# Performance work log

Measured on AMD Instinct MI355X. Metric: run time of the kernel, lower is better.

The kernel has to match this reference:

```python
import jax, jax.numpy as jnp
import numpy as np

B, T, IN, H, L, OUT = 2048, 512, 4, 64, 4, 5


def setup_inputs() -> dict:
    key = jax.random.key(0)
    ks = jax.random.split(key, 9)
    s = 0.1  # keep gates out of saturation
    return {
        "x": jax.random.normal(ks[0], (B, T, IN), jnp.float32),
        "W_ih0": jax.random.normal(ks[1], (4 * H, IN), jnp.float32) * s,
        "W_ih_r": jax.random.normal(ks[2], (L - 1, 4 * H, H), jnp.float32) * s,
        "W_hh": jax.random.normal(ks[3], (L, 4 * H, H), jnp.float32) * s,
        "b_ih": jax.random.normal(ks[4], (L, 4 * H), jnp.float32) * s,
        "b_hh": jax.random.normal(ks[5], (L, 4 * H), jnp.float32) * s,
        "W_fc": jax.random.normal(ks[6], (OUT, H), jnp.float32) * s,
        "b_fc": jax.random.normal(ks[7], (OUT,), jnp.float32) * s,
    }


def _lstm_layer(xs, W_ih, W_hh, b_ih, b_hh):
    # xs: [B, T, D_in] -> hs: [B, T, H]. PyTorch gate order: i, f, g, o.
    b, t = xs.shape[0], xs.shape[1]
    h_dim = W_hh.shape[1]
    # Precompute input contribution for all timesteps (one big GEMM).
    xg = jnp.einsum('btd,gd->btg', xs, W_ih) + b_ih  # [B, T, 4H]

    def step(carry, xg_t):
        h, c = carry
        g = xg_t + h @ W_hh.T + b_hh  # [B, 4H]
        i, f, gg, o = jnp.split(g, 4, axis=-1)
        c = jax.nn.sigmoid(f) * c + jax.nn.sigmoid(i) * jnp.tanh(gg)
        h = jax.nn.sigmoid(o) * jnp.tanh(c)
        return (h, c), h

    init = (jnp.zeros((b, h_dim), xs.dtype), jnp.zeros((b, h_dim), xs.dtype))
    (_, _), hs = jax.lax.scan(step, init, jnp.swapaxes(xg, 0, 1))  # hs: [T, B, H]
    return jnp.swapaxes(hs, 0, 1)


def reference(x, W_ih0, W_ih_r, W_hh, b_ih, b_hh, W_fc, b_fc):
    hs = _lstm_layer(x, W_ih0, W_hh[0], b_ih[0], b_hh[0])
    for l in range(1, L):
        hs = _lstm_layer(hs, W_ih_r[l - 1], W_hh[l], b_ih[l], b_hh[l])
    # fc on last timestep of top layer
    return hs[:, -1, :] @ W_fc.T + b_fc  # [B, OUT]
```

## Files before the change

kernel.cpp:

```cpp
#include <hip/hip_runtime.h>


#define B_    2048
#define T_    512
#define H_    64
#define OUT_  5
#define RSTR  136
#define LOG2E 1.44269504088896340736f

typedef _Float16 f16;
typedef __attribute__((ext_vector_type(8))) _Float16 f16x8;
typedef __attribute__((ext_vector_type(4))) float f32x4;

__device__ __forceinline__ float rcpf(float v) { return __builtin_amdgcn_rcpf(v); }
__device__ __forceinline__ float ex2(float v)  { return __builtin_amdgcn_exp2f(v); }

__global__ __launch_bounds__(1024, 4) void lstm_ring_k(
    const float* __restrict__ x,
    const float* __restrict__ W_ih0,
    const float* __restrict__ W_ihr,
    const float* __restrict__ W_hh,
    const float* __restrict__ b_ih,
    const float* __restrict__ b_hh,
    const float* __restrict__ W_fc,
    const float* __restrict__ b_fc,
    float* __restrict__ out)
{
    const int tid  = threadIdx.x;
    const int wave = tid >> 6;
    const int l    = wave >> 2;
    const int jj   = wave & 3;
    const int lane = tid & 63;
    const int q    = lane >> 4;
    const int ln   = lane & 15;
    const int u    = jj * 16 + ln;
    const int b0   = blockIdx.x * 8;

    __shared__ f16 buf[4][4][16][RSTR];
    __shared__ int flg[16];
    __shared__ float hf[8][H_ + 1];

    for (int k = tid; k < (int)(sizeof(buf) / 4); k += 1024) ((unsigned*)buf)[k] = 0u;
    if (tid < 16) flg[tid] = 0;

    const float* Whh = W_hh + (size_t)l * 256 * 64;
    const float* Wih = (l == 0) ? W_ih0 : (W_ihr + (size_t)(l - 1) * 256 * 64);
    const float scg[4] = {-LOG2E, -LOG2E, 2.0f * LOG2E, -LOG2E};

    f16x8 Wf[4][4];
    float biasv[4];
#pragma unroll
    for (int g4 = 0; g4 < 4; ++g4) {
        const int n = g4 * 64 + u;
        biasv[g4] = (b_ih[l * 256 + n] + b_hh[l * 256 + n]) * scg[g4];
#pragma unroll
        for (int kt = 0; kt < 4; ++kt) {
            f16x8 f;
#pragma unroll
            for (int e = 0; e < 8; ++e) {
                const int kap = kt * 32 + q * 8 + e;
                float wv;
                if (kap < 64) {
                    const int k = ((kap & 3) << 4) | (kap >> 2);
                    wv = Whh[n * 64 + k];
                } else {
                    const int kk = kap - 64;
                    if (l == 0) wv = (kk < 4) ? Wih[n * 4 + kk] : 0.0f;
                    else { const int k = ((kk & 3) << 4) | (kk >> 2); wv = Wih[n * 64 + k]; }
                }
                f[e] = (f16)(wv * scg[g4]);
            }
            Wf[g4][kt] = f;
        }
    }

    int fIdx = 0, fOff = 0;
    bool fUse = false;
    if (lane < 3)                             { fIdx = 4 * l + ((jj + 1 + lane) & 3); fOff = 0;  fUse = true; }
    else if (lane >= 3 && lane < 7 && l > 0)  { fIdx = 4 * (l - 1) + (lane - 3);      fOff = 1;  fUse = true; }
    else if (lane >= 7 && lane < 11 && l < 3) { fIdx = 4 * (l + 1) + (lane - 7);      fOff = -3; fUse = true; }

    const int l1 = (l < 3) ? l + 1 : 3;
    const int rdOff = ln * RSTR;
    const int owOff = 4 * q * RSTR + 4 * ln + jj;
    const int inOff = 4 * q * RSTR + 64 + 4 * ln + jj;

    const int xm = lane >> 2, xe = lane & 3;
    const int xrow = 4 * (xm >> 1) + (xm & 1);
    const bool xldr = (wave == 0 && lane < 32);
    float xA = 0.0f;

    __syncthreads();
    if (xldr) {
        const float x0 = x[(size_t)(b0 + xm) * (T_ * 4) + xe];
        buf[0][0][xrow][64 + xe] = (f16)x0;
        xA = x[(size_t)(b0 + xm) * (T_ * 4) + 4 + xe];
    }
    __syncthreads();

    const f32x4 Z0 = {0.f, 0.f, 0.f, 0.f};
    float cst[2] = {0.f, 0.f};

    auto body = [&](int t, int sl) {
        const int sn = (sl + 1) & 3;
        unsigned guard = 0;
        for (;;) {
            int v = 0x7fffffff;
            if (fUse) v = __hip_atomic_load(&flg[fIdx], __ATOMIC_ACQUIRE,
                                            __HIP_MEMORY_SCOPE_WORKGROUP);
            if (__all(v >= t + fOff)) break;
            if (++guard > 2) __builtin_amdgcn_s_sleep(1);
            if (guard > (1u << 16)) break;
        }

        const f16* rb = &buf[l][sl][0][0] + rdOff;
        f16x8 A[4];
#pragma unroll
        for (int kt = 0; kt < 4; ++kt)
            A[kt] = *(const f16x8*)(rb + kt * 32 + q * 8);

        f32x4 acc[4];
#pragma unroll
        for (int g4 = 0; g4 < 4; ++g4)
            acc[g4] = __builtin_amdgcn_mfma_f32_16x16x32_f16(A[0], Wf[g4][0], Z0, 0, 0, 0);
#pragma unroll
        for (int kt = 1; kt < 4; ++kt)
#pragma unroll
            for (int g4 = 0; g4 < 4; ++g4)
                acc[g4] = __builtin_amdgcn_mfma_f32_16x16x32_f16(A[kt], Wf[g4][kt], acc[g4], 0, 0, 0);

        if (xldr) {
            if (t + 1 < T_) buf[0][sn][xrow][64 + xe] = (f16)xA;
            if (t + 2 < T_) xA = x[(size_t)(b0 + xm) * (T_ * 4) + (t + 2) * 4 + xe];
        }

        f16* wO = &buf[l][sn][0][0] + owOff;
        f16* wI = &buf[l1][sl][0][0] + inOff;
#pragma unroll
        for (int rr = 0; rr < 2; ++rr) {
            const float si = rcpf(1.0f + ex2(acc[0][rr] + biasv[0]));
            const float sf = rcpf(1.0f + ex2(acc[1][rr] + biasv[1]));
            const float tg = 1.0f - 2.0f * rcpf(1.0f + ex2(acc[2][rr] + biasv[2]));
            const float so = rcpf(1.0f + ex2(acc[3][rr] + biasv[3]));
            const float c  = sf * cst[rr] + si * tg;
            cst[rr] = c;
            const float tc = 1.0f - 2.0f * rcpf(1.0f + ex2(c * (2.0f * LOG2E)));
            const float h  = so * tc;
            wO[rr * RSTR] = (f16)h;
            if (l < 3) wI[rr * RSTR] = (f16)h;
            if (l == 3 && t == T_ - 1) hf[2 * q + rr][u] = h;
        }

        if (lane == 0)
            __hip_atomic_store(&flg[wave], t + 1, __ATOMIC_RELEASE,
                               __HIP_MEMORY_SCOPE_WORKGROUP);
    };

#pragma unroll 1
    for (int t = 0; t < T_; t += 4) {
        body(t, 0);
        body(t + 1, 1);
        body(t + 2, 2);
        body(t + 3, 3);
    }

    __syncthreads();
    if (tid < 8 * OUT_) {
        const int b = tid / OUT_, o = tid % OUT_;
        float a = b_fc[o];
#pragma unroll
        for (int k = 0; k < H_; ++k)
            a = fmaf(hf[b][k], W_fc[o * H_ + k], a);
        out[(b0 + b) * OUT_ + o] = a;
    }
}

extern "C" void kernel_launch(void* const* d_in, const int* in_sizes, int n_in,
                              void* d_out, int out_size, void* d_ws, size_t ws_size,
                              hipStream_t stream) {
    const float* x     = (const float*)d_in[0];
    const float* W_ih0 = (const float*)d_in[1];
    const float* W_ihr = (const float*)d_in[2];
    const float* W_hh  = (const float*)d_in[3];
    const float* b_ih  = (const float*)d_in[4];
    const float* b_hh  = (const float*)d_in[5];
    const float* W_fc  = (const float*)d_in[6];
    const float* b_fc  = (const float*)d_in[7];
    float* out = (float*)d_out;

    lstm_ring_k<<<dim3(B_ / 8), dim3(1024), 0, stream>>>(
        x, W_ih0, W_ihr, W_hh, b_ih, b_hh, W_fc, b_fc, out);
}
```

Before: 602.9 us.

## Replace flag-based layer ring with skewed wavefront using block barriers

Replaces per-wave atomic flag spinning with a diagonal (skewed) schedule where layer l processes timestep i-l and all waves synchronize with __syncthreads each step, double-buffering hidden state per layer. The whole x sequence for the block is preloaded into LDS as fp16 up front, and layer 0 skips the fourth MFMA k-tile since its input has only 4 features. This aims to remove spin-wait and atomic overhead and per-step global x loads, at the cost of a full workgroup barrier every step, 3 extra pipeline fill/drain steps, and larger LDS usage that may reduce occupancy.

```diff
diff --git a/kernel.cpp b/kernel.cpp
--- a/kernel.cpp
+++ b/kernel.cpp
@@ -5,17 +5,18 @@
 #define T_    512
 #define H_    64
 #define OUT_  5
-#define RSTR  136
+#define RSTR  72
 #define LOG2E 1.44269504088896340736f
 
 typedef _Float16 f16;
+typedef __attribute__((ext_vector_type(4))) _Float16 f16x4;
 typedef __attribute__((ext_vector_type(8))) _Float16 f16x8;
 typedef __attribute__((ext_vector_type(4))) float f32x4;
 
 __device__ __forceinline__ float rcpf(float v) { return __builtin_amdgcn_rcpf(v); }
 __device__ __forceinline__ float ex2(float v)  { return __builtin_amdgcn_exp2f(v); }
 
-__global__ __launch_bounds__(1024, 4) void lstm_ring_k(
+__global__ __launch_bounds__(1024, 4) void lstm_skew_k(
     const float* __restrict__ x,
     const float* __restrict__ W_ih0,
     const float* __restrict__ W_ihr,
@@ -36,12 +37,20 @@
     const int u    = jj * 16 + ln;
     const int b0   = blockIdx.x * 8;
 
-    __shared__ f16 buf[4][4][16][RSTR];
-    __shared__ int flg[16];
+    __shared__ f16  buf[4][2][16][RSTR];
+    __shared__ f16  xlds[T_ * 32];
     __shared__ float hf[8][H_ + 1];
 
     for (int k = tid; k < (int)(sizeof(buf) / 4); k += 1024) ((unsigned*)buf)[k] = 0u;
-    if (tid < 16) flg[tid] = 0;
+
+#pragma unroll
+    for (int k = 0; k < 4; ++k) {
+        const int idx = tid + k * 1024;
+        const int bb  = idx >> 9, tt = idx & 511;
+        const float4 v = *(const float4*)(x + (size_t)(b0 + bb) * (T_ * 4) + tt * 4);
+        f16x4 h4; h4[0] = (f16)v.x; h4[1] = (f16)v.y; h4[2] = (f16)v.z; h4[3] = (f16)v.w;
+        *(f16x4*)&xlds[tt * 32 + bb * 4] = h4;
+    }
 
     const float* Whh = W_hh + (size_t)l * 256 * 64;
     const float* Wih = (l == 0) ? W_ih0 : (W_ihr + (size_t)(l - 1) * 256 * 64);
@@ -74,97 +83,82 @@
         }
     }
 
-    int fIdx = 0, fOff = 0;
-    bool fUse = false;
-    if (lane < 3)                             { fIdx = 4 * l + ((jj + 1 + lane) & 3); fOff = 0;  fUse = true; }
-    else if (lane >= 3 && lane < 7 && l > 0)  { fIdx = 4 * (l - 1) + (lane - 3);      fOff = 1;  fUse = true; }
-    else if (lane >= 7 && lane < 11 && l < 3) { fIdx = 4 * (l + 1) + (lane - 7);      fOff = -3; fUse = true; }
+    const int rdOff = ln * RSTR;
+    const f16* hRd0 = &buf[l][0][0][0] + rdOff;
+    const f16* hRd1 = &buf[l][1][0][0] + rdOff;
+    const int  lp   = (l > 0) ? (l - 1) : 0;
+    const f16* iRd0 = &buf[lp][0][0][0] + rdOff;
+    const f16* iRd1 = &buf[lp][1][0][0] + rdOff;
+    const int owOff = 4 * q * RSTR + 4 * ln + jj;
+    f16* hWr0 = &buf[l][0][0][0] + owOff;
+    f16* hWr1 = &buf[l][1][0][0] + owOff;
 
-    const int l1 = (l < 3) ? l + 1 : 3;
-    const int rdOff = ln * RSTR;
-    const int owOff = 4 * q * RSTR + 4 * ln + jj;
-    const int inOff = 4 * q * RSTR + 64 + 4 * ln + jj;
+    const int  xb  = 2 * (ln >> 2) + (ln & 1);
+    const bool xok = (l == 0) && (q == 0) && ((ln & 2) == 0);
+    const f16* xP  = &xlds[xb * 4];
 
-    const int xm = lane >> 2, xe = lane & 3;
-    const int xrow = 4 * (xm >> 1) + (xm & 1);
-    const bool xldr = (wave == 0 && lane < 32);
-    float xA = 0.0f;
-
-    __syncthreads();
-    if (xldr) {
-        const float x0 = x[(size_t)(b0 + xm) * (T_ * 4) + xe];
-        buf[0][0][xrow][64 + xe] = (f16)x0;
-        xA = x[(size_t)(b0 + xm) * (T_ * 4) + 4 + xe];
-    }
     __syncthreads();
 
     const f32x4 Z0 = {0.f, 0.f, 0.f, 0.f};
     float cst[2] = {0.f, 0.f};
 
-    auto body = [&](int t, int sl) {
-        const int sn = (sl + 1) & 3;
-        unsigned guard = 0;
-        for (;;) {
-            int v = 0x7fffffff;
-            if (fUse) v = __hip_atomic_load(&flg[fIdx], __ATOMIC_ACQUIRE,
-                                            __HIP_MEMORY_SCOPE_WORKGROUP);
-            if (__all(v >= t + fOff)) break;
-            if (++guard > 2) __builtin_amdgcn_s_sleep(1);
-            if (guard > (1u << 16)) break;
-        }
+    auto step = [&](const int i, const f16* hb, const f16* ib, f16* wOb) {
+        const int t = i - l;
+        if ((unsigned)t < T_) {
+            f16x8 A0 = *(const f16x8*)(hb + q * 8);
+            f16x8 A1 = *(const f16x8*)(hb + 32 + q * 8);
+            f16x8 A2;
+            if (l == 0) {
+#pragma unroll
+                for (int e = 0; e < 8; ++e) A2[e] = (f16)0;
+                if (xok) {
+                    const f16x4 xv = *(const f16x4*)(xP + t * 32);
+                    A2[0] = xv[0]; A2[1] = xv[1]; A2[2] = xv[2]; A2[3] = xv[3];
+                }
+            } else {
+                A2 = *(const f16x8*)(ib + q * 8);
+            }
 
-        const f16* rb = &buf[l][sl][0][0] + rdOff;
-        f16x8 A[4];
-#pragma unroll
-        for (int kt = 0; kt < 4; ++kt)
-            A[kt] = *(const f16x8*)(rb + kt * 32 + q * 8);
-
-        f32x4 acc[4];
-#pragma unroll
-        for (int g4 = 0; g4 < 4; ++g4)
-            acc[g4] = __builtin_amdgcn_mfma_f32_16x16x32_f16(A[0], Wf[g4][0], Z0, 0, 0, 0);
-#pragma unroll
-        for (int kt = 1; kt < 4; ++kt)
+            f32x4 acc[4];
 #pragma unroll
             for (int g4 = 0; g4 < 4; ++g4)
-                acc[g4] = __builtin_amdgcn_mfma_f32_16x16x32_f16(A[kt], Wf[g4][kt], acc[g4], 0, 0, 0);
+                acc[g4] = __builtin_amdgcn_mfma_f32_16x16x32_f16(A0, Wf[g4][0], Z0, 0, 0, 0);
+#pragma unroll
+            for (int g4 = 0; g4 < 4; ++g4)
+                acc[g4] = __builtin_amdgcn_mfma_f32_16x16x32_f16(A1, Wf[g4][1], acc[g4], 0, 0, 0);
+#pragma unroll
+            for (int g4 = 0; g4 < 4; ++g4)
+                acc[g4] = __builtin_amdgcn_mfma_f32_16x16x32_f16(A2, Wf[g4][2], acc[g4], 0, 0, 0);
+            if (l != 0) {
+                const f16x8 A3 = *(const f16x8*)(ib + 32 + q * 8);
+#pragma unroll
+                for (int g4 = 0; g4 < 4; ++g4)
+                    acc[g4] = __builtin_amdgcn_mfma_f32_16x16x32_f16(A3, Wf[g4][3], acc[g4], 0, 0, 0);
+            }
 
-        if (xldr) {
-            if (t + 1 < T_) buf[0][sn][xrow][64 + xe] = (f16)xA;
-            if (t + 2 < T_) xA = x[(size_t)(b0 + xm) * (T_ * 4) + (t + 2) * 4 + xe];
+#pragma unroll
+            for (int rr = 0; rr < 2; ++rr) {
+                const float si = rcpf(1.0f + ex2(acc[0][rr] + biasv[0]));
+                const float sf = rcpf(1.0f + ex2(acc[1][rr] + biasv[1]));
+                const float tg = 1.0f - 2.0f * rcpf(1.0f + ex2(acc[2][rr] + biasv[2]));
+                const float so = rcpf(1.0f + ex2(acc[3][rr] + biasv[3]));
+                const float c  = sf * cst[rr] + si * tg;
+                cst[rr] = c;
+                const float tc = 1.0f - 2.0f * rcpf(1.0f + ex2(c * (2.0f * LOG2E)));
+                const float h  = so * tc;
+                wOb[rr * RSTR] = (f16)h;
+                if (l == 3 && t == T_ - 1) hf[2 * q + rr][u] = h;
+            }
         }
-
-        f16* wO = &buf[l][sn][0][0] + owOff;
-        f16* wI = &buf[l1][sl][0][0] + inOff;
-#pragma unroll
-        for (int rr = 0; rr < 2; ++rr) {
-            const float si = rcpf(1.0f + ex2(acc[0][rr] + biasv[0]));
-            const float sf = rcpf(1.0f + ex2(acc[1][rr] + biasv[1]));
-            const float tg = 1.0f - 2.0f * rcpf(1.0f + ex2(acc[2][rr] + biasv[2]));
-            const float so = rcpf(1.0f + ex2(acc[3][rr] + biasv[3]));
-            const float c  = sf * cst[rr] + si * tg;
-            cst[rr] = c;
-            const float tc = 1.0f - 2.0f * rcpf(1.0f + ex2(c * (2.0f * LOG2E)));
-            const float h  = so * tc;
-            wO[rr * RSTR] = (f16)h;
-            if (l < 3) wI[rr * RSTR] = (f16)h;
-            if (l == 3 && t == T_ - 1) hf[2 * q + rr][u] = h;
-        }
-
-        if (lane == 0)
-            __hip_atomic_store(&flg[wave], t + 1, __ATOMIC_RELEASE,
-                               __HIP_MEMORY_SCOPE_WORKGROUP);
+        __syncthreads();
     };
 
 #pragma unroll 1
-    for (int t = 0; t < T_; t += 4) {
-        body(t, 0);
-        body(t + 1, 1);
-        body(t + 2, 2);
-        body(t + 3, 3);
+    for (int i = 0; i < 516; i += 2) {
+        step(i,     hRd0, iRd0, hWr1);
+        step(i + 1, hRd1, iRd1, hWr0);
     }
 
-    __syncthreads();
     if (tid < 8 * OUT_) {
         const int b = tid / OUT_, o = tid % OUT_;
         float a = b_fc[o];
@@ -188,6 +182,6 @@
     const float* b_fc  = (const float*)d_in[7];
     float* out = (float*)d_out;
 
-    lstm_ring_k<<<dim3(B_ / 8), dim3(1024), 0, stream>>>(
+    lstm_skew_k<<<dim3(B_ / 8), dim3(1024), 0, stream>>>(
         x, W_ih0, W_ihr, W_hh, b_ih, b_hh, W_fc, b_fc, out);
 }
```

Measured after the change: 639.0 us. 1.06x slower.
